# Optimization experiments

Hardware: AMD Instinct MI355X
Metric: run time of the kernel (lower is better)

The kernel has to match this reference:

```python
import jax, jax.numpy as jnp
import numpy as np

N = 100000          # nodes
E = 3200000         # edges (before self-loops)
F_IN = 500          # Pubmed feature dim
H1, C1 = 8, 8       # layer-1 heads, channels per head
H2, C2 = 1, 7       # layer-2 heads, channels (num classes)
NEG_SLOPE = 0.2


def _glorot(key, shape, fan_in):
    return jax.random.normal(key, shape, dtype=jnp.float32) / np.sqrt(fan_in)


def setup_inputs() -> dict:
    key = jax.random.key(0)
    ks = jax.random.split(key, 10)
    x = jax.random.normal(ks[0], (N, F_IN), dtype=jnp.float32)
    edge_index = jax.random.randint(ks[1], (2, E), 0, N, dtype=jnp.int64)
    W1 = _glorot(ks[2], (F_IN, H1 * C1), F_IN)
    a_src1 = _glorot(ks[3], (H1, C1), C1)
    a_dst1 = _glorot(ks[4], (H1, C1), C1)
    b1 = jnp.zeros((H1 * C1,), dtype=jnp.float32)
    W2 = _glorot(ks[5], (H1 * C1, H2 * C2), H1 * C1)
    a_src2 = _glorot(ks[6], (H2, C2), C2)
    a_dst2 = _glorot(ks[7], (H2, C2), C2)
    b2 = jnp.zeros((H2 * C2,), dtype=jnp.float32)
    return {"x": x, "edge_index": edge_index, "W1": W1, "a_src1": a_src1,
            "a_dst1": a_dst1, "b1": b1, "W2": W2, "a_src2": a_src2,
            "a_dst2": a_dst2, "b2": b2}


def gat_conv(x, src, dst, W, a_src, a_dst, bias, heads, out_ch):
    # x: [N, F_in]; src/dst: [E'] (self-loops included); returns [N, heads*out_ch]
    h = (x @ W).reshape(N, heads, out_ch)                      # [N, H, C]
    alpha_s = jnp.einsum('nhc,hc->nh', h, a_src)               # [N, H]
    alpha_d = jnp.einsum('nhc,hc->nh', h, a_dst)               # [N, H]
    e = alpha_s[src] + alpha_d[dst]                            # [E', H]
    e = jax.nn.leaky_relu(e, NEG_SLOPE)
    # segment softmax over incoming edges of each dst node
    m = jax.ops.segment_max(e, dst, num_segments=N)            # [N, H]
    ex = jnp.exp(e - m[dst])                                   # [E', H]
    denom = jax.ops.segment_sum(ex, dst, num_segments=N)       # [N, H]
    alpha = ex / denom[dst]                                    # [E', H]
    msg = alpha[:, :, None] * h[src]                           # [E', H, C]
    out = jax.ops.segment_sum(msg, dst, num_segments=N)        # [N, H, C]
    return out.reshape(N, heads * out_ch) + bias


def reference(x, edge_index, W1, a_src1, a_dst1, b1, W2, a_src2, a_dst2, b2):
    loops = jnp.arange(N, dtype=edge_index.dtype)
    src = jnp.concatenate([edge_index[0], loops])
    dst = jnp.concatenate([edge_index[1], loops])
    h = gat_conv(x, src, dst, W1, a_src1, a_dst1, b1, H1, C1)   # [N, 64]
    out = gat_conv(h, src, dst, W2, a_src2, a_dst2, b2, H2, C2) # [N, 7]
    return jax.nn.log_softmax(out, axis=1)
```

## Files before the change

kernel.cpp:

```cpp
#include <hip/hip_runtime.h>
#include <hip/hip_bf16.h>
#include <hip/hip_fp16.h>

#define N_NODES 100000
#define N_EDGES 3200000
#define ET (N_EDGES + N_NODES)
#define F_IN 500
#define H1 8
#define C1 8
#define F1 64
#define C2 7

#define BSH 6
#define NB ((N_NODES + 63) / 64)
#define CAP 6144
#define FB 64
#define FCHUNK ((ET + FB - 1) / FB)

typedef __attribute__((ext_vector_type(8))) short short8;
typedef __attribute__((ext_vector_type(4))) float f32x4;

__device__ __forceinline__ unsigned short f2bf(float f) {
    const unsigned u = __float_as_uint(f);
    return (unsigned short)((u + 0x7FFFu + ((u >> 16) & 1u)) >> 16);
}

__global__ __launch_bounds__(1024) void fill_count(const int* __restrict__ ei,
                                                   int* __restrict__ cntmat) {
    __shared__ int hist[NB];
    const int t = threadIdx.x, blk = blockIdx.x;
    for (int i = t; i < NB; i += 1024) hist[i] = 0;
    __syncthreads();
    const int s0 = blk * FCHUNK;
    const int s1 = min(s0 + FCHUNK, ET);
    for (int i = s0 + t; i < s1; i += 1024) {
        const int dst = (i < N_EDGES) ? ei[N_EDGES + i] : (i - N_EDGES);
        atomicAdd(&hist[dst >> BSH], 1);
    }
    __syncthreads();
    int* row = cntmat + (size_t)blk * NB;
    for (int i = t; i < NB; i += 1024) row[i] = hist[i];
}

__global__ __launch_bounds__(1024) void scan2(const int* __restrict__ cntmat,
                                              int* __restrict__ boff,
                                              int* __restrict__ basemat,
                                              int* __restrict__ rowptr) {
    __shared__ int tot[2048];
    __shared__ int wsum[16];
    const int t = threadIdx.x;
    const int lane = t & 63;
    const int w = t >> 6;
    for (int b = t; b < 2048; b += 1024) {
        int s = 0;
        if (b < NB)
            for (int j = 0; j < FB; ++j) s += cntmat[(size_t)j * NB + b];
        tot[b] = s;
    }
    __syncthreads();
    int running = 0;
    for (int t0 = 0; t0 < 2048; t0 += 1024) {
        const int v = tot[t0 + t];
        int sc = v;
#pragma unroll
        for (int d = 1; d < 64; d <<= 1) {
            int u = __shfl_up(sc, d);
            if (lane >= d) sc += u;
        }
        if (lane == 63) wsum[w] = sc;
        __syncthreads();
        if (t < 16) {
            int ws = wsum[t];
#pragma unroll
            for (int d = 1; d < 16; d <<= 1) {
                int u = __shfl_up(ws, d);
                if (t >= d) ws += u;
            }
            wsum[t] = ws;
        }
        __syncthreads();
        const int excl = running + (w ? wsum[w - 1] : 0) + sc - v;
        if (t0 + t < NB) boff[t0 + t] = excl;
        const int tt = wsum[15];
        __syncthreads();
        tot[t0 + t] = excl;
        running += tt;
    }
    if (t == 0) {
        boff[NB] = running;
        rowptr[N_NODES] = running;
    }
    __syncthreads();
    for (int b = t; b < NB; b += 1024) {
        int run = tot[b];
        for (int j = 0; j < FB; ++j) {
            basemat[(size_t)j * NB + b] = run;
            run += cntmat[(size_t)j * NB + b];
        }
    }
}

__global__ __launch_bounds__(1024) void fill_scatter(const int* __restrict__ ei,
                                                     const int* __restrict__ basemat,
                                                     unsigned int* __restrict__ ebuf) {
    __shared__ int cur[NB];
    const int t = threadIdx.x, blk = blockIdx.x;
    const int* row = basemat + (size_t)blk * NB;
    for (int i = t; i < NB; i += 1024) cur[i] = row[i];
    __syncthreads();
    const int s0 = blk * FCHUNK;
    const int s1 = min(s0 + FCHUNK, ET);
    for (int i = s0 + t; i < s1; i += 1024) {
        int src, dst;
        if (i < N_EDGES) { src = ei[i]; dst = ei[N_EDGES + i]; }
        else             { src = dst = i - N_EDGES; }
        const int b = dst >> BSH;
        const int p = atomicAdd(&cur[b], 1);
        ebuf[p] = (unsigned)src | ((unsigned)(dst & 63) << 17);
    }
}

__global__ __launch_bounds__(256) void bucket_csr(const int* __restrict__ boff,
                                                  const unsigned int* __restrict__ ebuf,
                                                  int* __restrict__ col,
                                                  int* __restrict__ rowptr) {
    __shared__ unsigned int ebs[CAP];
    __shared__ int colb[CAP];
    __shared__ int hist[64], curs[64];
    const int b = blockIdx.x, t = threadIdx.x;
    const int e0 = boff[b], e1 = boff[b + 1];
    const int cnt = e1 - e0;
    if (t < 64) hist[t] = 0;
    __syncthreads();

    if (cnt <= CAP) {
        for (int i = t; i < cnt; i += 256) {
            const unsigned v = ebuf[e0 + i];
            ebs[i] = v;
            atomicAdd(&hist[v >> 17], 1);
        }
        __syncthreads();
        if (t < 64) {
            const int v = hist[t];
            int sc = v;
#pragma unroll
            for (int d = 1; d < 64; d <<= 1) {
                int u = __shfl_up(sc, d);
                if (t >= d) sc += u;
            }
            const int excl = sc - v;
            curs[t] = excl;
            const int n = (b << BSH) + t;
            if (n < N_NODES) rowptr[n] = e0 + excl;
        }
        __syncthreads();
        for (int i = t; i < cnt; i += 256) {
            const unsigned v = ebs[i];
            const int p = atomicAdd(&curs[v >> 17], 1);
            colb[p] = (int)(v & 0x1FFFFu);
        }
        __syncthreads();
        for (int i = t; i < cnt; i += 256) col[e0 + i] = colb[i];
    } else {
        for (int i = t; i < cnt; i += 256) atomicAdd(&hist[ebuf[e0 + i] >> 17], 1);
        __syncthreads();
        if (t < 64) {
            const int v = hist[t];
            int sc = v;
#pragma unroll
            for (int d = 1; d < 64; d <<= 1) {
                int u = __shfl_up(sc, d);
                if (t >= d) sc += u;
            }
            const int excl = sc - v;
            curs[t] = excl;
            const int n = (b << BSH) + t;
            if (n < N_NODES) rowptr[n] = e0 + excl;
        }
        __syncthreads();
        for (int i = t; i < cnt; i += 256) {
            const unsigned v = ebuf[e0 + i];
            const int p = atomicAdd(&curs[v >> 17], 1);
            col[e0 + p] = (int)(v & 0x1FFFFu);
        }
    }
}

__global__ __launch_bounds__(256) void wprep(const float* __restrict__ W1,
                                             short* __restrict__ wpk) {
    const int idx = blockIdx.x * 256 + threadIdx.x;
    if (idx >= 32768) return;
    const int j = idx & 7;
    const int l = (idx >> 3) & 63;
    const int f = (idx >> 9) & 3;
    const int ks = idx >> 11;
    const int k = ks * 32 + ((l >> 4) << 3) + j;
    const int col = f * 16 + (l & 15);
    const float fv = (k < F_IN) ? W1[k * F1 + col] : 0.f;
    wpk[idx] = (short)f2bf(fv);
}

__global__ __launch_bounds__(256) void gemm1_kernel(
    const float* __restrict__ x, const short* __restrict__ wpk,
    const float* __restrict__ a_src, const float* __restrict__ a_dst,
    __half* __restrict__ h1, float* __restrict__ as1, float* __restrict__ ad1)
{
    const int t = threadIdx.x;
    const int l = t & 63;
    const int w = t >> 6;
    const int row0 = blockIdx.x * 64 + w * 16;
    const int r = l & 15;
    const int koff = (l >> 4) * 8;
    const float* __restrict__ xp =
        x + (size_t)min(row0 + r, N_NODES - 1) * F_IN + koff;
    const short* __restrict__ wl = wpk + (l << 3);

    f32x4 acc[4];
#pragma unroll
    for (int f = 0; f < 4; ++f) acc[f] = (f32x4){0.f, 0.f, 0.f, 0.f};

    float4 va = *(const float4*)(xp);
    float4 vb = *(const float4*)(xp + 4);
    short8 bcur[4];
#pragma unroll
    for (int f = 0; f < 4; ++f)
        bcur[f] = *(const short8*)(wl + (f << 9));

    for (int ks = 0; ks < 16; ++ks) {
        float v[8];
        v[0] = va.x; v[1] = va.y; v[2] = va.z; v[3] = va.w;
        v[4] = vb.x; v[5] = vb.y; v[6] = vb.z; v[7] = vb.w;
        if (ks < 14) {
            va = *(const float4*)(xp + (ks + 1) * 32);
            vb = *(const float4*)(xp + (ks + 1) * 32 + 4);
        } else if (ks == 14) {
            float tv[8];
#pragma unroll
            for (int j = 0; j < 8; ++j)
                tv[j] = (koff + j < 20) ? xp[480 + j] : 0.f;
            va = make_float4(tv[0], tv[1], tv[2], tv[3]);
            vb = make_float4(tv[4], tv[5], tv[6], tv[7]);
        }
        short8 bnext[4];
        if (ks < 15) {
#pragma unroll
            for (int f = 0; f < 4; ++f)
                bnext[f] = *(const short8*)(wl + (((ks + 1) * 4 + f) << 9));
        }
        short8 ah, al;
#pragma unroll
        for (int j = 0; j < 8; ++j) {
            const unsigned short h = f2bf(v[j]);
            ah[j] = (short)h;
            al[j] = (short)f2bf(v[j] - __uint_as_float((unsigned)h << 16));
        }
#pragma unroll
        for (int f = 0; f < 4; ++f) {
            acc[f] = __builtin_amdgcn_mfma_f32_16x16x32_bf16(ah, bcur[f], acc[f], 0, 0, 0);
            acc[f] = __builtin_amdgcn_mfma_f32_16x16x32_bf16(al, bcur[f], acc[f], 0, 0, 0);
        }
        if (ks < 15) {
#pragma unroll
            for (int f = 0; f < 4; ++f) bcur[f] = bnext[f];
        }
    }

    const int g = l >> 4;
    const int p = r >> 3;
    float asv[4], adv[4];
#pragma unroll
    for (int f = 0; f < 4; ++f) {
        asv[f] = a_src[f * 16 + r];
        adv[f] = a_dst[f * 16 + r];
    }
#pragma unroll
    for (int f = 0; f < 4; ++f) {
#pragma unroll
        for (int reg = 0; reg < 4; ++reg) {
            const int row = row0 + g * 4 + reg;
            const float hv = acc[f][reg];
            if (row < N_NODES)
                h1[(size_t)row * F1 + f * 16 + r] = __float2half(hv);
            float ps = hv * asv[f];
            float pd = hv * adv[f];
            ps += __shfl_xor(ps, 1); ps += __shfl_xor(ps, 2); ps += __shfl_xor(ps, 4);
            pd += __shfl_xor(pd, 1); pd += __shfl_xor(pd, 2); pd += __shfl_xor(pd, 4);
            if ((l & 7) == 0 && row < N_NODES) {
                as1[row * H1 + f * 2 + p] = ps;
                ad1[row * H1 + f * 2 + p] = pd;
            }
        }
    }
}

__global__ __launch_bounds__(256) void agg1_kernel(
    const int* __restrict__ rowptr, const int* __restrict__ col,
    const __half* __restrict__ h1, const float* __restrict__ as1,
    const float* __restrict__ ad1, const float* __restrict__ b1,
    float* __restrict__ hout)
{
    const int l = threadIdx.x & 63;
    const int n = (blockIdx.x << 2) + (threadIdx.x >> 6);
    if (n >= N_NODES) return;
    const int jsub = l & 7;
    const int hsub = l >> 3;
    const int pbase = l & 56;
    const int r0 = rowptr[n], r1 = rowptr[n + 1];
    const float adh = ad1[(n << 3) + hsub];

    float denom = 0.f, acc = 0.f;
    int j0 = r0;
    for (; j0 + 8 <= r1; j0 += 8) {
        const int s_l = col[j0 + jsub];
        float e = as1[(s_l << 3) + hsub] + adh;
        e = fmaxf(e, 0.2f * e);
        const float p_l = __expf(e);
#pragma unroll
        for (int j = 0; j < 8; ++j) {
            const float p = __shfl(p_l, pbase + j);
            const int s_j = __builtin_amdgcn_readlane(s_l, j);
            const float v = __half2float(h1[((size_t)(unsigned)s_j << 6) + l]);
            denom += p;
            acc = fmaf(p, v, acc);
        }
    }
    if (j0 < r1) {
        const int jc = min(j0 + jsub, r1 - 1);
        const int s_l = col[jc];
        float e = as1[(s_l << 3) + hsub] + adh;
        e = fmaxf(e, 0.2f * e);
        const float p_l = __expf(e);
#pragma unroll
        for (int j = 0; j < 8; ++j) {
            if (j0 + j < r1) {
                const float p = __shfl(p_l, pbase + j);
                const int s_j = __builtin_amdgcn_readlane(s_l, j);
                const float v = __half2float(h1[((size_t)(unsigned)s_j << 6) + l]);
                denom += p;
                acc = fmaf(p, v, acc);
            }
        }
    }
    hout[(n << 6) + l] = acc / denom + b1[l];
}

__global__ __launch_bounds__(256) void gemm2_kernel(
    const float* __restrict__ hin, const float* __restrict__ W2,
    const float* __restrict__ a_src, const float* __restrict__ a_dst,
    float* __restrict__ h2p, float* __restrict__ as2, float* __restrict__ ad2)
{
    __shared__ float w2s[F1 * C2];
    __shared__ float as_s[C2], ad_s[C2];
    for (int i = threadIdx.x; i < F1 * C2; i += blockDim.x) w2s[i] = W2[i];
    if (threadIdx.x < C2) { as_s[threadIdx.x] = a_src[threadIdx.x]; ad_s[threadIdx.x] = a_dst[threadIdx.x]; }
    __syncthreads();

    int n = blockIdx.x * blockDim.x + threadIdx.x;
    if (n >= N_NODES) return;
    float acc[C2];
#pragma unroll
    for (int c = 0; c < C2; ++c) acc[c] = 0.f;
    const float* hp = hin + (size_t)n * F1;
    for (int k = 0; k < F1; k += 4) {
        const float4 hv = *(const float4*)(hp + k);
#pragma unroll
        for (int c = 0; c < C2; ++c) {
            acc[c] = fmaf(hv.x, w2s[(k + 0) * C2 + c], acc[c]);
            acc[c] = fmaf(hv.y, w2s[(k + 1) * C2 + c], acc[c]);
            acc[c] = fmaf(hv.z, w2s[(k + 2) * C2 + c], acc[c]);
            acc[c] = fmaf(hv.w, w2s[(k + 3) * C2 + c], acc[c]);
        }
    }
    float s = 0.f, d = 0.f;
#pragma unroll
    for (int c = 0; c < C2; ++c) {
        s = fmaf(acc[c], as_s[c], s);
        d = fmaf(acc[c], ad_s[c], d);
    }
    float4* o = (float4*)(h2p + (size_t)n * 8);
    o[0] = make_float4(acc[0], acc[1], acc[2], acc[3]);
    o[1] = make_float4(acc[4], acc[5], acc[6], 0.f);
    as2[n] = s;
    ad2[n] = d;
}

__global__ __launch_bounds__(256) void agg2_kernel(
    const int* __restrict__ rowptr, const int* __restrict__ col,
    const float* __restrict__ h2p, const float* __restrict__ as2,
    const float* __restrict__ ad2, const float* __restrict__ b2,
    float* __restrict__ out)
{
    const int gq = (blockIdx.x * 256 + threadIdx.x) >> 2;
    const int q = threadIdx.x & 3;
    if (gq >= N_NODES) return;
    const int r0 = rowptr[gq], r1 = rowptr[gq + 1];
    const float adn = ad2[gq];

    float denom = 0.f;
    float a0 = 0, a1 = 0, a2 = 0, a3 = 0, a4 = 0, a5 = 0, a6 = 0;
    for (int j = r0 + q; j < r1; j += 4) {
        const int s = col[j];
        float e = as2[s] + adn;
        e = fmaxf(e, 0.2f * e);
        const float ex = __expf(e);
        const float4 va = *(const float4*)(h2p + (size_t)s * 8);
        const float4 vb = *(const float4*)(h2p + (size_t)s * 8 + 4);
        denom += ex;
        a0 = fmaf(ex, va.x, a0); a1 = fmaf(ex, va.y, a1);
        a2 = fmaf(ex, va.z, a2); a3 = fmaf(ex, va.w, a3);
        a4 = fmaf(ex, vb.x, a4); a5 = fmaf(ex, vb.y, a5);
        a6 = fmaf(ex, vb.z, a6);
    }
#pragma unroll
    for (int d = 1; d < 4; d <<= 1) {
        denom += __shfl_xor(denom, d);
        a0 += __shfl_xor(a0, d); a1 += __shfl_xor(a1, d);
        a2 += __shfl_xor(a2, d); a3 += __shfl_xor(a3, d);
        a4 += __shfl_xor(a4, d); a5 += __shfl_xor(a5, d);
        a6 += __shfl_xor(a6, d);
    }
    const float inv = 1.f / denom;
    float v0 = a0 * inv + b2[0], v1 = a1 * inv + b2[1];
    float v2 = a2 * inv + b2[2], v3 = a3 * inv + b2[3];
    float v4 = a4 * inv + b2[4], v5 = a5 * inv + b2[5];
    float v6 = a6 * inv + b2[6];
    float mx = fmaxf(fmaxf(fmaxf(v0, v1), fmaxf(v2, v3)), fmaxf(fmaxf(v4, v5), v6));
    const float se = __expf(v0 - mx) + __expf(v1 - mx) + __expf(v2 - mx) +
                     __expf(v3 - mx) + __expf(v4 - mx) + __expf(v5 - mx) +
                     __expf(v6 - mx);
    const float lse = __logf(se) + mx;
    const float wa = (q == 0) ? v0 : (q == 1) ? v1 : (q == 2) ? v2 : v3;
    const float wb = (q == 0) ? v4 : (q == 1) ? v5 : v6;
    out[gq * C2 + q] = wa - lse;
    if (q < 3) out[gq * C2 + q + 4] = wb - lse;
}

extern "C" void kernel_launch(void* const* d_in, const int* in_sizes, int n_in,
                              void* d_out, int out_size, void* d_ws, size_t ws_size,
                              hipStream_t stream) {
    const float* x      = (const float*)d_in[0];
    const int*   ei     = (const int*)  d_in[1];
    const float* W1     = (const float*)d_in[2];
    const float* a_src1 = (const float*)d_in[3];
    const float* a_dst1 = (const float*)d_in[4];
    const float* b1     = (const float*)d_in[5];
    const float* W2     = (const float*)d_in[6];
    const float* a_src2 = (const float*)d_in[7];
    const float* a_dst2 = (const float*)d_in[8];
    const float* b2     = (const float*)d_in[9];
    float* out = (float*)d_out;

    char* ws = (char*)d_ws;
    size_t off = 0;
    auto alloc = [&](size_t bytes) -> void* {
        void* p = ws + off;
        off += (bytes + 255) & ~(size_t)255;
        return p;
    };
    int*    rowptr  = (int*)   alloc((N_NODES + 1) * sizeof(int));
    int*    boff    = (int*)   alloc((size_t)(NB + 1) * sizeof(int));
    int*    cntmat  = (int*)   alloc((size_t)FB * NB * sizeof(int));
    int*    basemat = (int*)   alloc((size_t)FB * NB * sizeof(int));
    int*    colidx  = (int*)   alloc((size_t)ET * sizeof(int));
    short*  wpk     = (short*) alloc((size_t)32768 * sizeof(short));
    __half* h1      = (__half*)alloc((size_t)N_NODES * F1 * sizeof(__half));
    float*  as1     = (float*) alloc((size_t)N_NODES * H1 * sizeof(float));
    float*  ad1     = (float*) alloc((size_t)N_NODES * H1 * sizeof(float));
    float*  hout1   = (float*) alloc((size_t)N_NODES * F1 * sizeof(float));
    float*  h2p     = (float*) alloc((size_t)N_NODES * 8 * sizeof(float));
    float*  as2     = (float*) alloc((size_t)N_NODES * sizeof(float));
    float*  ad2     = (float*) alloc((size_t)N_NODES * sizeof(float));
    unsigned int* ebuf = (unsigned int*)hout1;

    wprep<<<128, 256, 0, stream>>>(W1, wpk);
    fill_count<<<FB, 1024, 0, stream>>>(ei, cntmat);
    scan2<<<1, 1024, 0, stream>>>(cntmat, boff, basemat, rowptr);
    fill_scatter<<<FB, 1024, 0, stream>>>(ei, basemat, ebuf);
    bucket_csr<<<NB, 256, 0, stream>>>(boff, ebuf, colidx, rowptr);
    gemm1_kernel<<<(N_NODES + 63) / 64, 256, 0, stream>>>(x, wpk, a_src1, a_dst1, h1, as1, ad1);
    agg1_kernel<<<(N_NODES + 3) / 4, 256, 0, stream>>>(rowptr, colidx, h1, as1, ad1, b1, hout1);
    gemm2_kernel<<<(N_NODES + 255) / 256, 256, 0, stream>>>(hout1, W2, a_src2, a_dst2, h2p, as2, ad2);
    agg2_kernel<<<(N_NODES * 4 + 255) / 256, 256, 0, stream>>>(rowptr, colidx, h2p, as2, ad2, b2, out);
}
```

Baseline: 384.6 us.

## Fuse per-bucket CSR construction into both aggregation kernels, drop bucket_csr

Removes the separate bucket_csr pass and the global col/rowptr arrays. Each aggregation block now rebuilds its 64-node bucket's local CSR in shared memory from the bucketed edge buffer, then aggregates with one wave handling 16 nodes (agg1) or 4 threads per node (agg2). The fill block count also doubles from 64 to 128. This saves a kernel launch and a global write and read of the column array, but the local sort is done twice and agg1 now runs only NB blocks, each walking 16 nodes serially per wave, which reduces parallelism.

```diff
diff --git a/kernel.cpp b/kernel.cpp
--- a/kernel.cpp
+++ b/kernel.cpp
@@ -13,8 +13,8 @@
 
 #define BSH 6
 #define NB ((N_NODES + 63) / 64)
-#define CAP 6144
-#define FB 64
+#define CAP2 4096
+#define FB 128
 #define FCHUNK ((ET + FB - 1) / FB)
 
 typedef __attribute__((ext_vector_type(8))) short short8;
@@ -44,8 +44,7 @@
 
 __global__ __launch_bounds__(1024) void scan2(const int* __restrict__ cntmat,
                                               int* __restrict__ boff,
-                                              int* __restrict__ basemat,
-                                              int* __restrict__ rowptr) {
+                                              int* __restrict__ basemat) {
     __shared__ int tot[2048];
     __shared__ int wsum[16];
     const int t = threadIdx.x;
@@ -86,10 +85,7 @@
         tot[t0 + t] = excl;
         running += tt;
     }
-    if (t == 0) {
-        boff[NB] = running;
-        rowptr[N_NODES] = running;
-    }
+    if (t == 0) boff[NB] = running;
     __syncthreads();
     for (int b = t; b < NB; b += 1024) {
         int run = tot[b];
@@ -117,72 +113,6 @@
         const int b = dst >> BSH;
         const int p = atomicAdd(&cur[b], 1);
         ebuf[p] = (unsigned)src | ((unsigned)(dst & 63) << 17);
-    }
-}
-
-__global__ __launch_bounds__(256) void bucket_csr(const int* __restrict__ boff,
-                                                  const unsigned int* __restrict__ ebuf,
-                                                  int* __restrict__ col,
-                                                  int* __restrict__ rowptr) {
-    __shared__ unsigned int ebs[CAP];
-    __shared__ int colb[CAP];
-    __shared__ int hist[64], curs[64];
-    const int b = blockIdx.x, t = threadIdx.x;
-    const int e0 = boff[b], e1 = boff[b + 1];
-    const int cnt = e1 - e0;
-    if (t < 64) hist[t] = 0;
-    __syncthreads();
-
-    if (cnt <= CAP) {
-        for (int i = t; i < cnt; i += 256) {
-            const unsigned v = ebuf[e0 + i];
-            ebs[i] = v;
-            atomicAdd(&hist[v >> 17], 1);
-        }
-        __syncthreads();
-        if (t < 64) {
-            const int v = hist[t];
-            int sc = v;
-#pragma unroll
-            for (int d = 1; d < 64; d <<= 1) {
-                int u = __shfl_up(sc, d);
-                if (t >= d) sc += u;
-            }
-            const int excl = sc - v;
-            curs[t] = excl;
-            const int n = (b << BSH) + t;
-            if (n < N_NODES) rowptr[n] = e0 + excl;
-        }
-        __syncthreads();
-        for (int i = t; i < cnt; i += 256) {
-            const unsigned v = ebs[i];
-            const int p = atomicAdd(&curs[v >> 17], 1);
-            colb[p] = (int)(v & 0x1FFFFu);
-        }
-        __syncthreads();
-        for (int i = t; i < cnt; i += 256) col[e0 + i] = colb[i];
-    } else {
-        for (int i = t; i < cnt; i += 256) atomicAdd(&hist[ebuf[e0 + i] >> 17], 1);
-        __syncthreads();
-        if (t < 64) {
-            const int v = hist[t];
-            int sc = v;
-#pragma unroll
-            for (int d = 1; d < 64; d <<= 1) {
-                int u = __shfl_up(sc, d);
-                if (t >= d) sc += u;
-            }
-            const int excl = sc - v;
-            curs[t] = excl;
-            const int n = (b << BSH) + t;
-            if (n < N_NODES) rowptr[n] = e0 + excl;
-        }
-        __syncthreads();
-        for (int i = t; i < cnt; i += 256) {
-            const unsigned v = ebuf[e0 + i];
-            const int p = atomicAdd(&curs[v >> 17], 1);
-            col[e0 + p] = (int)(v & 0x1FFFFu);
-        }
     }
 }
 
@@ -294,54 +224,111 @@
 }
 
 __global__ __launch_bounds__(256) void agg1_kernel(
-    const int* __restrict__ rowptr, const int* __restrict__ col,
+    const int* __restrict__ boff, const unsigned int* __restrict__ ebuf,
     const __half* __restrict__ h1, const float* __restrict__ as1,
     const float* __restrict__ ad1, const float* __restrict__ b1,
     float* __restrict__ hout)
 {
-    const int l = threadIdx.x & 63;
-    const int n = (blockIdx.x << 2) + (threadIdx.x >> 6);
-    if (n >= N_NODES) return;
-    const int jsub = l & 7;
-    const int hsub = l >> 3;
-    const int pbase = l & 56;
-    const int r0 = rowptr[n], r1 = rowptr[n + 1];
-    const float adh = ad1[(n << 3) + hsub];
-
-    float denom = 0.f, acc = 0.f;
-    int j0 = r0;
-    for (; j0 + 8 <= r1; j0 += 8) {
-        const int s_l = col[j0 + jsub];
-        float e = as1[(s_l << 3) + hsub] + adh;
-        e = fmaxf(e, 0.2f * e);
-        const float p_l = __expf(e);
-#pragma unroll
-        for (int j = 0; j < 8; ++j) {
-            const float p = __shfl(p_l, pbase + j);
-            const int s_j = __builtin_amdgcn_readlane(s_l, j);
-            const float v = __half2float(h1[((size_t)(unsigned)s_j << 6) + l]);
-            denom += p;
-            acc = fmaf(p, v, acc);
-        }
-    }
-    if (j0 < r1) {
-        const int jc = min(j0 + jsub, r1 - 1);
-        const int s_l = col[jc];
-        float e = as1[(s_l << 3) + hsub] + adh;
-        e = fmaxf(e, 0.2f * e);
-        const float p_l = __expf(e);
-#pragma unroll
-        for (int j = 0; j < 8; ++j) {
-            if (j0 + j < r1) {
-                const float p = __shfl(p_l, pbase + j);
-                const int s_j = __builtin_amdgcn_readlane(s_l, j);
-                const float v = __half2float(h1[((size_t)(unsigned)s_j << 6) + l]);
-                denom += p;
-                acc = fmaf(p, v, acc);
-            }
-        }
-    }
-    hout[(n << 6) + l] = acc / denom + b1[l];
+    __shared__ int colb[CAP2];
+    __shared__ int hist[64], curs[64], rowp[65];
+    const int t = threadIdx.x, b = blockIdx.x;
+    const int e0 = boff[b];
+    const int cnt = boff[b + 1] - e0;
+    const int l = t & 63;
+    const int w = t >> 6;
+    if (t < 64) hist[t] = 0;
+    __syncthreads();
+
+    if (cnt <= CAP2) {
+        for (int i = t; i < cnt; i += 256)
+            atomicAdd(&hist[ebuf[e0 + i] >> 17], 1);
+        __syncthreads();
+        if (t < 64) {
+            const int v = hist[t];
+            int sc = v;
+#pragma unroll
+            for (int d = 1; d < 64; d <<= 1) {
+                int u = __shfl_up(sc, d);
+                if (t >= d) sc += u;
+            }
+            rowp[t] = sc - v;
+            curs[t] = sc - v;
+            if (t == 63) rowp[64] = sc;
+        }
+        __syncthreads();
+        for (int i = t; i < cnt; i += 256) {
+            const unsigned v = ebuf[e0 + i];
+            const int p = atomicAdd(&curs[v >> 17], 1);
+            colb[p] = (int)(v & 0x1FFFFu);
+        }
+        __syncthreads();
+
+        const int jsub = l & 7;
+        const int hsub = l >> 3;
+        const int pbase = l & 56;
+        for (int ni = 0; ni < 16; ++ni) {
+            const int d = w * 16 + ni;
+            const int n = (b << 6) + d;
+            if (n >= N_NODES) break;
+            const int rr0 = rowp[d], rr1 = rowp[d + 1];
+            const float adh = ad1[(n << 3) + hsub];
+            float den = 0.f, acc = 0.f;
+            int j0 = rr0;
+            for (; j0 + 8 <= rr1; j0 += 8) {
+                const int s_l = colb[j0 + jsub];
+                float e = as1[(s_l << 3) + hsub] + adh;
+                e = fmaxf(e, 0.2f * e);
+                const float p_l = __expf(e);
+#pragma unroll
+                for (int j = 0; j < 8; ++j) {
+                    const float p = __shfl(p_l, pbase + j);
+                    const int s_j = __builtin_amdgcn_readlane(s_l, j);
+                    const float v = __half2float(h1[((size_t)(unsigned)s_j << 6) + l]);
+                    den += p;
+                    acc = fmaf(p, v, acc);
+                }
+            }
+            if (j0 < rr1) {
+                const int s_l = colb[min(j0 + jsub, rr1 - 1)];
+                float e = as1[(s_l << 3) + hsub] + adh;
+                e = fmaxf(e, 0.2f * e);
+                const float p_l = __expf(e);
+#pragma unroll
+                for (int j = 0; j < 8; ++j) {
+                    if (j0 + j < rr1) {
+                        const float p = __shfl(p_l, pbase + j);
+                        const int s_j = __builtin_amdgcn_readlane(s_l, j);
+                        const float v = __half2float(h1[((size_t)(unsigned)s_j << 6) + l]);
+                        den += p;
+                        acc = fmaf(p, v, acc);
+                    }
+                }
+            }
+            hout[((size_t)n << 6) + l] = acc / den + b1[l];
+        }
+    } else {
+        const int hsub = l >> 3;
+        for (int ni = 0; ni < 16; ++ni) {
+            const int d = w * 16 + ni;
+            const int n = (b << 6) + d;
+            if (n >= N_NODES) break;
+            const float adh = ad1[(n << 3) + hsub];
+            float den = 0.f, acc = 0.f;
+            for (int i = 0; i < cnt; ++i) {
+                const unsigned v = ebuf[e0 + i];
+                if ((int)(v >> 17) == d) {
+                    const int s = (int)(v & 0x1FFFFu);
+                    float e = as1[(s << 3) + hsub] + adh;
+                    e = fmaxf(e, 0.2f * e);
+                    const float p = __expf(e);
+                    const float hv = __half2float(h1[((size_t)s << 6) + l]);
+                    den += p;
+                    acc = fmaf(p, hv, acc);
+                }
+            }
+            hout[((size_t)n << 6) + l] = acc / den + b1[l];
+        }
+    }
 }
 
 __global__ __launch_bounds__(256) void gemm2_kernel(
@@ -385,54 +372,131 @@
 }
 
 __global__ __launch_bounds__(256) void agg2_kernel(
-    const int* __restrict__ rowptr, const int* __restrict__ col,
+    const int* __restrict__ boff, const unsigned int* __restrict__ ebuf,
     const float* __restrict__ h2p, const float* __restrict__ as2,
     const float* __restrict__ ad2, const float* __restrict__ b2,
     float* __restrict__ out)
 {
-    const int gq = (blockIdx.x * 256 + threadIdx.x) >> 2;
-    const int q = threadIdx.x & 3;
-    if (gq >= N_NODES) return;
-    const int r0 = rowptr[gq], r1 = rowptr[gq + 1];
-    const float adn = ad2[gq];
-
-    float denom = 0.f;
-    float a0 = 0, a1 = 0, a2 = 0, a3 = 0, a4 = 0, a5 = 0, a6 = 0;
-    for (int j = r0 + q; j < r1; j += 4) {
-        const int s = col[j];
-        float e = as2[s] + adn;
-        e = fmaxf(e, 0.2f * e);
-        const float ex = __expf(e);
-        const float4 va = *(const float4*)(h2p + (size_t)s * 8);
-        const float4 vb = *(const float4*)(h2p + (size_t)s * 8 + 4);
-        denom += ex;
-        a0 = fmaf(ex, va.x, a0); a1 = fmaf(ex, va.y, a1);
-        a2 = fmaf(ex, va.z, a2); a3 = fmaf(ex, va.w, a3);
-        a4 = fmaf(ex, vb.x, a4); a5 = fmaf(ex, vb.y, a5);
-        a6 = fmaf(ex, vb.z, a6);
-    }
-#pragma unroll
-    for (int d = 1; d < 4; d <<= 1) {
-        denom += __shfl_xor(denom, d);
-        a0 += __shfl_xor(a0, d); a1 += __shfl_xor(a1, d);
-        a2 += __shfl_xor(a2, d); a3 += __shfl_xor(a3, d);
-        a4 += __shfl_xor(a4, d); a5 += __shfl_xor(a5, d);
-        a6 += __shfl_xor(a6, d);
-    }
-    const float inv = 1.f / denom;
-    float v0 = a0 * inv + b2[0], v1 = a1 * inv + b2[1];
-    float v2 = a2 * inv + b2[2], v3 = a3 * inv + b2[3];
-    float v4 = a4 * inv + b2[4], v5 = a5 * inv + b2[5];
-    float v6 = a6 * inv + b2[6];
-    float mx = fmaxf(fmaxf(fmaxf(v0, v1), fmaxf(v2, v3)), fmaxf(fmaxf(v4, v5), v6));
-    const float se = __expf(v0 - mx) + __expf(v1 - mx) + __expf(v2 - mx) +
-                     __expf(v3 - mx) + __expf(v4 - mx) + __expf(v5 - mx) +
-                     __expf(v6 - mx);
-    const float lse = __logf(se) + mx;
-    const float wa = (q == 0) ? v0 : (q == 1) ? v1 : (q == 2) ? v2 : v3;
-    const float wb = (q == 0) ? v4 : (q == 1) ? v5 : v6;
-    out[gq * C2 + q] = wa - lse;
-    if (q < 3) out[gq * C2 + q + 4] = wb - lse;
+    __shared__ int colb[CAP2];
+    __shared__ int hist[64], curs[64], rowp[65];
+    const int t = threadIdx.x, b = blockIdx.x;
+    const int e0 = boff[b];
+    const int cnt = boff[b + 1] - e0;
+    if (t < 64) hist[t] = 0;
+    __syncthreads();
+
+    const int d = t >> 2;
+    const int q = t & 3;
+    const int n = (b << 6) + d;
+
+    if (cnt <= CAP2) {
+        for (int i = t; i < cnt; i += 256)
+            atomicAdd(&hist[ebuf[e0 + i] >> 17], 1);
+        __syncthreads();
+        if (t < 64) {
+            const int v = hist[t];
+            int sc = v;
+#pragma unroll
+            for (int dd = 1; dd < 64; dd <<= 1) {
+                int u = __shfl_up(sc, dd);
+                if (t >= dd) sc += u;
+            }
+            rowp[t] = sc - v;
+            curs[t] = sc - v;
+            if (t == 63) rowp[64] = sc;
+        }
+        __syncthreads();
+        for (int i = t; i < cnt; i += 256) {
+            const unsigned v = ebuf[e0 + i];
+            const int p = atomicAdd(&curs[v >> 17], 1);
+            colb[p] = (int)(v & 0x1FFFFu);
+        }
+        __syncthreads();
+
+        if (n >= N_NODES) return;
+        const int rr0 = rowp[d], rr1 = rowp[d + 1];
+        const float adn = ad2[n];
+        float denom = 0.f;
+        float a0 = 0, a1 = 0, a2 = 0, a3 = 0, a4 = 0, a5 = 0, a6 = 0;
+        for (int j = rr0 + q; j < rr1; j += 4) {
+            const int s = colb[j];
+            float e = as2[s] + adn;
+            e = fmaxf(e, 0.2f * e);
+            const float ex = __expf(e);
+            const float4 va = *(const float4*)(h2p + (size_t)s * 8);
+            const float4 vb = *(const float4*)(h2p + (size_t)s * 8 + 4);
+            denom += ex;
+            a0 = fmaf(ex, va.x, a0); a1 = fmaf(ex, va.y, a1);
+            a2 = fmaf(ex, va.z, a2); a3 = fmaf(ex, va.w, a3);
+            a4 = fmaf(ex, vb.x, a4); a5 = fmaf(ex, vb.y, a5);
+            a6 = fmaf(ex, vb.z, a6);
+        }
+#pragma unroll
+        for (int dd = 1; dd < 4; dd <<= 1) {
+            denom += __shfl_xor(denom, dd);
+            a0 += __shfl_xor(a0, dd); a1 += __shfl_xor(a1, dd);
+            a2 += __shfl_xor(a2, dd); a3 += __shfl_xor(a3, dd);
+            a4 += __shfl_xor(a4, dd); a5 += __shfl_xor(a5, dd);
+            a6 += __shfl_xor(a6, dd);
+        }
+        const float inv = 1.f / denom;
+        float v0 = a0 * inv + b2[0], v1 = a1 * inv + b2[1];
+        float v2 = a2 * inv + b2[2], v3 = a3 * inv + b2[3];
+        float v4 = a4 * inv + b2[4], v5 = a5 * inv + b2[5];
+        float v6 = a6 * inv + b2[6];
+        float mx = fmaxf(fmaxf(fmaxf(v0, v1), fmaxf(v2, v3)), fmaxf(fmaxf(v4, v5), v6));
+        const float se = __expf(v0 - mx) + __expf(v1 - mx) + __expf(v2 - mx) +
+                         __expf(v3 - mx) + __expf(v4 - mx) + __expf(v5 - mx) +
+                         __expf(v6 - mx);
+        const float lse = __logf(se) + mx;
+        const float wa = (q == 0) ? v0 : (q == 1) ? v1 : (q == 2) ? v2 : v3;
+        const float wb = (q == 0) ? v4 : (q == 1) ? v5 : v6;
+        out[n * C2 + q] = wa - lse;
+        if (q < 3) out[n * C2 + q + 4] = wb - lse;
+    } else {
+        if (n >= N_NODES) return;
+        const float adn = ad2[n];
+        float denom = 0.f;
+        float a0 = 0, a1 = 0, a2 = 0, a3 = 0, a4 = 0, a5 = 0, a6 = 0;
+        for (int i = q; i < cnt; i += 4) {
+            const unsigned v = ebuf[e0 + i];
+            if ((int)(v >> 17) == d) {
+                const int s = (int)(v & 0x1FFFFu);
+                float e = as2[s] + adn;
+                e = fmaxf(e, 0.2f * e);
+                const float ex = __expf(e);
+                const float4 va = *(const float4*)(h2p + (size_t)s * 8);
+                const float4 vb = *(const float4*)(h2p + (size_t)s * 8 + 4);
+                denom += ex;
+                a0 = fmaf(ex, va.x, a0); a1 = fmaf(ex, va.y, a1);
+                a2 = fmaf(ex, va.z, a2); a3 = fmaf(ex, va.w, a3);
+                a4 = fmaf(ex, vb.x, a4); a5 = fmaf(ex, vb.y, a5);
+                a6 = fmaf(ex, vb.z, a6);
+            }
+        }
+#pragma unroll
+        for (int dd = 1; dd < 4; dd <<= 1) {
+            denom += __shfl_xor(denom, dd);
+            a0 += __shfl_xor(a0, dd); a1 += __shfl_xor(a1, dd);
+            a2 += __shfl_xor(a2, dd); a3 += __shfl_xor(a3, dd);
+            a4 += __shfl_xor(a4, dd); a5 += __shfl_xor(a5, dd);
+            a6 += __shfl_xor(a6, dd);
+        }
+        const float inv = 1.f / denom;
+        float v0 = a0 * inv + b2[0], v1 = a1 * inv + b2[1];
+        float v2 = a2 * inv + b2[2], v3 = a3 * inv + b2[3];
+        float v4 = a4 * inv + b2[4], v5 = a5 * inv + b2[5];
+        float v6 = a6 * inv + b2[6];
+        float mx = fmaxf(fmaxf(fmaxf(v0, v1), fmaxf(v2, v3)), fmaxf(fmaxf(v4, v5), v6));
+        const float se = __expf(v0 - mx) + __expf(v1 - mx) + __expf(v2 - mx) +
+                         __expf(v3 - mx) + __expf(v4 - mx) + __expf(v5 - mx) +
+                         __expf(v6 - mx);
+        const float lse = __logf(se) + mx;
+        const float wa = (q == 0) ? v0 : (q == 1) ? v1 : (q == 2) ? v2 : v3;
+        const float wb = (q == 0) ? v4 : (q == 1) ? v5 : v6;
+        out[n * C2 + q] = wa - lse;
+        if (q < 3) out[n * C2 + q + 4] = wb - lse;
+    }
 }
 
 extern "C" void kernel_launch(void* const* d_in, const int* in_sizes, int n_in,
@@ -457,28 +521,25 @@
         off += (bytes + 255) & ~(size_t)255;
         return p;
     };
-    int*    rowptr  = (int*)   alloc((N_NODES + 1) * sizeof(int));
-    int*    boff    = (int*)   alloc((size_t)(NB + 1) * sizeof(int));
-    int*    cntmat  = (int*)   alloc((size_t)FB * NB * sizeof(int));
-    int*    basemat = (int*)   alloc((size_t)FB * NB * sizeof(int));
-    int*    colidx  = (int*)   alloc((size_t)ET * sizeof(int));
-    short*  wpk     = (short*) alloc((size_t)32768 * sizeof(short));
-    __half* h1      = (__half*)alloc((size_t)N_NODES * F1 * sizeof(__half));
-    float*  as1     = (float*) alloc((size_t)N_NODES * H1 * sizeof(float));
-    float*  ad1     = (float*) alloc((size_t)N_NODES * H1 * sizeof(float));
-    float*  hout1   = (float*) alloc((size_t)N_NODES * F1 * sizeof(float));
-    float*  h2p     = (float*) alloc((size_t)N_NODES * 8 * sizeof(float));
-    float*  as2     = (float*) alloc((size_t)N_NODES * sizeof(float));
-    float*  ad2     = (float*) alloc((size_t)N_NODES * sizeof(float));
-    unsigned int* ebuf = (unsigned int*)hout1;
+    int*          boff    = (int*)   alloc((size_t)(NB + 1) * sizeof(int));
+    int*          cntmat  = (int*)   alloc((size_t)FB * NB * sizeof(int));
+    int*          basemat = (int*)   alloc((size_t)FB * NB * sizeof(int));
+    unsigned int* ebuf    = (unsigned int*)alloc((size_t)ET * sizeof(unsigned int));
+    short*        wpk     = (short*) alloc((size_t)32768 * sizeof(short));
+    __half*       h1      = (__half*)alloc((size_t)N_NODES * F1 * sizeof(__half));
+    float*        as1     = (float*) alloc((size_t)N_NODES * H1 * sizeof(float));
+    float*        ad1     = (float*) alloc((size_t)N_NODES * H1 * sizeof(float));
+    float*        hout1   = (float*) alloc((size_t)N_NODES * F1 * sizeof(float));
+    float*        h2p     = (float*) alloc((size_t)N_NODES * 8 * sizeof(float));
+    float*        as2     = (float*) alloc((size_t)N_NODES * sizeof(float));
+    float*        ad2     = (float*) alloc((size_t)N_NODES * sizeof(float));
 
     wprep<<<128, 256, 0, stream>>>(W1, wpk);
     fill_count<<<FB, 1024, 0, stream>>>(ei, cntmat);
-    scan2<<<1, 1024, 0, stream>>>(cntmat, boff, basemat, rowptr);
+    scan2<<<1, 1024, 0, stream>>>(cntmat, boff, basemat);
     fill_scatter<<<FB, 1024, 0, stream>>>(ei, basemat, ebuf);
-    bucket_csr<<<NB, 256, 0, stream>>>(boff, ebuf, colidx, rowptr);
     gemm1_kernel<<<(N_NODES + 63) / 64, 256, 0, stream>>>(x, wpk, a_src1, a_dst1, h1, as1, ad1);
-    agg1_kernel<<<(N_NODES + 3) / 4, 256, 0, stream>>>(rowptr, colidx, h1, as1, ad1, b1, hout1);
+    agg1_kernel<<<NB, 256, 0, stream>>>(boff, ebuf, h1, as1, ad1, b1, hout1);
     gemm2_kernel<<<(N_NODES + 255) / 256, 256, 0, stream>>>(hout1, W2, a_src2, a_dst2, h2p, as2, ad2);
-    agg2_kernel<<<(N_NODES * 4 + 255) / 256, 256, 0, stream>>>(rowptr, colidx, h2p, as2, ad2, b2, out);
-}
+    agg2_kernel<<<NB, 256, 0, stream>>>(boff, ebuf, h2p, as2, ad2, b2, out);
+}
```

Result: faster. 336.5 us (median of 2 runs) (-12.5%).
